# Kernel tuning notes

Measured on AMD Instinct MI355X. Metric: run time of the kernel, lower is better.

Reference implementation:

```python
import jax, jax.numpy as jnp
import numpy as np

BN_EPS = 1e-5

def bn(x, gamma, beta):
    # x: [N, C]; BatchNorm2d over (batch, spatial) == node axis here (training-mode batch stats)
    mu = x.mean(axis=0, keepdims=True)
    var = x.var(axis=0, keepdims=True)
    return (x - mu) * jax.lax.rsqrt(var + BN_EPS) * gamma + beta

def octree_conv(x, neigh, W):
    # x: [N, Cin]; neigh: [N, K] with values in [0, N], N == empty neighbor
    # W: [K, Cin, Cout]. Sparse octree conv = neighbor gather + contraction.
    xp = jnp.concatenate([x, jnp.zeros((1, x.shape[1]), x.dtype)], axis=0)  # zero row for empties
    g = xp[neigh]                                  # [N, K, Cin]
    return jnp.einsum('nkc,kcd->nd', g, W)         # [N, Cout]

def setup_inputs() -> dict:
    key = jax.random.key(0)
    ks = jax.random.split(key, 8)
    N, Cin, Cout, Cb, K = 60000, 256, 512, 128, 27
    s = 0.05
    return {
        'x': jax.random.normal(ks[0], (1, Cin, N, 1), jnp.float32),
        'neigh': jax.random.randint(ks[1], (N, K), 0, N + 1),
        'W1a': jax.random.normal(ks[2], (Cb, Cin), jnp.float32) * s,
        'g1a': jnp.ones((Cb,), jnp.float32), 'b1a': jnp.zeros((Cb,), jnp.float32),
        'W3': jax.random.normal(ks[3], (K, Cb, Cb), jnp.float32) * s,
        'g3': jnp.ones((Cb,), jnp.float32), 'b3': jnp.zeros((Cb,), jnp.float32),
        'W1b': jax.random.normal(ks[4], (Cout, Cb), jnp.float32) * s,
        'g1b': jnp.ones((Cout,), jnp.float32), 'b1b': jnp.zeros((Cout,), jnp.float32),
        'Wc': jax.random.normal(ks[5], (Cout, Cin), jnp.float32) * s,
        'gc': jnp.ones((Cout,), jnp.float32), 'bc': jnp.zeros((Cout,), jnp.float32),
    }

def reference(x, neigh, W1a, g1a, b1a, W3, g3, b3, W1b, g1b, b1b, Wc, gc, bc):
    h = jnp.squeeze(x, axis=(0, 3)).T                         # [N, Cin]
    c1 = jax.nn.relu(bn(h @ W1a.T, g1a, b1a))                 # 1x1 conv + BN + ReLU -> [N, Cb]
    c2 = jax.nn.relu(bn(octree_conv(c1, neigh, W3), g3, b3))  # sparse 3x3 octree conv + BN + ReLU
    c3 = bn(c2 @ W1b.T, g1b, b1b)                             # 1x1 conv + BN -> [N, Cout]
    sc = bn(h @ Wc.T, gc, bc)                                 # shortcut 1x1 conv + BN (Cin != Cout)
    out = jax.nn.relu(c3 + sc)
    return out.T[None, :, :, None]                            # [1, Cout, N, 1]
```

## Files before the change

kernel.cpp:

```cpp
#include <hip/hip_runtime.h>


typedef __bf16 bf16x8 __attribute__((ext_vector_type(8)));
typedef float f32x4 __attribute__((ext_vector_type(4)));
typedef unsigned short u16x8 __attribute__((ext_vector_type(8)));
typedef unsigned short u16x4 __attribute__((ext_vector_type(4)));

__device__ __forceinline__ unsigned short f2bfu(float f) {
  union { float f; unsigned u; } v; v.f = f;
  unsigned r = v.u + 0x7fffu + ((v.u >> 16) & 1u);
  return (unsigned short)(r >> 16);
}
__device__ __forceinline__ float bfu2f(unsigned short s) {
  union { unsigned u; float f; } v; v.u = ((unsigned)s) << 16;
  return v.f;
}

__device__ __forceinline__ void gload_lds16(const unsigned short* g, unsigned short* l) {
  __builtin_amdgcn_global_load_lds(
      (const __attribute__((address_space(1))) unsigned int*)(unsigned long long)g,
      (__attribute__((address_space(3))) unsigned int*)(unsigned int)(unsigned long long)l,
      16, 0, 0);
}

__device__ __forceinline__ int xcd_swz(int bid, int nwg) {
  int q = nwg >> 3, r = nwg & 7;
  int xcd = bid & 7, idx = bid >> 3;
  int base = xcd < r ? xcd * (q + 1) : r * (q + 1) + (xcd - r) * q;
  return base + idx;
}

__global__ __launch_bounds__(256) void prep_transpose(
    const float* __restrict__ x, unsigned short* __restrict__ h,
    const float* __restrict__ W1a, const float* __restrict__ W3,
    const float* __restrict__ W1b, const float* __restrict__ Wc,
    unsigned short* __restrict__ w1a, unsigned short* __restrict__ w3t,
    unsigned short* __restrict__ w1b, unsigned short* __restrict__ wc,
    int M, int MT) {
  __shared__ float tile[64][65];
  int t = threadIdx.x;
  if (blockIdx.x < 432) {
    int i = blockIdx.x * 256 + t;
    for (; i < 442368; i += 432 * 256) {
      if (i < 32768)  w1a[i] = f2bfu(W1a[i]);
      if (i < 65536)  w1b[i] = f2bfu(W1b[i]);
      if (i < 131072) wc[i]  = f2bfu(Wc[i]);
      int k = i >> 14, rr = i & 16383;
      int d = rr >> 7, c = rr & 127;
      w3t[i] = f2bfu(W3[(k << 14) + (c << 7) + d]);
    }
    return;
  }
  int bid = blockIdx.x - 432;
  int n0 = (bid % MT) * 64, c0 = (bid / MT) * 64;
  int nl = t & 63;
#pragma unroll
  for (int i = 0; i < 16; ++i) {
    int cl = i * 4 + (t >> 6);
    int n = n0 + nl;
    tile[cl][nl] = (n < M) ? x[(size_t)(c0 + cl) * M + n] : 0.f;
  }
  __syncthreads();
  int cl = t & 63;
#pragma unroll
  for (int i = 0; i < 16; ++i) {
    int nl2 = i * 4 + (t >> 6);
    int n = n0 + nl2;
    h[(size_t)n * 256 + c0 + cl] = f2bfu(tile[cl][nl2]);
  }
}

__global__ __launch_bounds__(512, 4) void gemm128(
    const unsigned short* __restrict__ A, const unsigned short* __restrict__ W,
    unsigned short* __restrict__ C, float* __restrict__ partials,
    int M, int Kd, int Nc, int ncol) {
  __shared__ unsigned short sA[2][128 * 64];
  __shared__ unsigned short sB[2][128 * 64];
  __shared__ float sStat[8][2][128];
  int t = threadIdx.x, wave = t >> 6, lane = t & 63;
  int flat = xcd_swz(blockIdx.x, gridDim.x);
  int n0 = (flat % ncol) * 128;
  int rowt = flat / ncol;
  int m0 = rowt * 128;
  int wr = wave >> 1, wcc = wave & 1;
  int l4 = lane >> 4, lc = lane & 15, lc7 = lc & 7;
  int lrow = lane >> 3, lch = lane & 7;
  f32x4 acc[2][4] = {};
  const int np = Kd >> 6;

  auto STAGE = [&](int p, int buf) {
    int k0 = p << 6;
#pragma unroll
    for (int i = 0; i < 2; ++i) {
      int row = wave * 16 + i * 8 + lrow;
      int sc = lch ^ (row & 7);
      gload_lds16(A + (size_t)(m0 + row) * Kd + k0 + sc * 8, &sA[buf][(wave * 16 + i * 8) * 64]);
    }
#pragma unroll
    for (int i = 0; i < 2; ++i) {
      int row = wave * 16 + i * 8 + lrow;
      int sc = lch ^ (row & 7);
      gload_lds16(W + (size_t)(n0 + row) * Kd + k0 + sc * 8, &sB[buf][(wave * 16 + i * 8) * 64]);
    }
  };
  auto COMPUTE = [&](int buf) {
#pragma unroll
    for (int kk = 0; kk < 2; ++kk) {
      bf16x8 af[2], bfr[4];
#pragma unroll
      for (int mi = 0; mi < 2; ++mi) {
        int row = wr * 32 + mi * 16 + lc;
        int chunk = (kk * 4 + l4) ^ lc7;
        af[mi] = __builtin_bit_cast(bf16x8, *(const u16x8*)(&sA[buf][row * 64 + chunk * 8]));
      }
#pragma unroll
      for (int ni = 0; ni < 4; ++ni) {
        int row = wcc * 64 + ni * 16 + lc;
        int chunk = (kk * 4 + l4) ^ lc7;
        bfr[ni] = __builtin_bit_cast(bf16x8, *(const u16x8*)(&sB[buf][row * 64 + chunk * 8]));
      }
      __builtin_amdgcn_s_setprio(1);
#pragma unroll
      for (int mi = 0; mi < 2; ++mi)
#pragma unroll
        for (int ni = 0; ni < 4; ++ni)
          acc[mi][ni] = __builtin_amdgcn_mfma_f32_16x16x32_bf16(af[mi], bfr[ni], acc[mi][ni], 0, 0, 0);
      __builtin_amdgcn_s_setprio(0);
    }
  };

  STAGE(0, 0);
  for (int p = 0; p < np; ++p) {
    int cur = p & 1;
    if (p < np - 1) {
      STAGE(p + 1, cur ^ 1);
      asm volatile("s_waitcnt vmcnt(4)" ::: "memory");
    } else {
      asm volatile("s_waitcnt vmcnt(0)" ::: "memory");
    }
    __builtin_amdgcn_sched_barrier(0);
    __builtin_amdgcn_s_barrier();
    __builtin_amdgcn_sched_barrier(0);
    COMPUTE(cur);
    __builtin_amdgcn_sched_barrier(0);
    __builtin_amdgcn_s_barrier();
  }

#pragma unroll
  for (int ni = 0; ni < 4; ++ni) {
    float s = 0.f, q = 0.f;
    int col = wcc * 64 + ni * 16 + lc;
#pragma unroll
    for (int mi = 0; mi < 2; ++mi)
#pragma unroll
      for (int j = 0; j < 4; ++j) {
        int n = m0 + wr * 32 + mi * 16 + l4 * 4 + j;
        unsigned short u = f2bfu(acc[mi][ni][j]);
        if (n < M) C[(size_t)n * Nc + n0 + col] = u;
        float v = bfu2f(u);
        s += v; q += v * v;
      }
    s += __shfl_xor(s, 16); s += __shfl_xor(s, 32);
    q += __shfl_xor(q, 16); q += __shfl_xor(q, 32);
    if (lane < 16) {
      sStat[wave][0][col] = s;
      sStat[wave][1][col] = q;
    }
  }
  __syncthreads();
  if (t < 128) {
    int wcs = t >> 6;
    float s = 0.f, q = 0.f;
#pragma unroll
    for (int g = 0; g < 4; ++g) {
      s += sStat[g * 2 + wcs][0][t];
      q += sStat[g * 2 + wcs][1][t];
    }
    partials[(size_t)rowt * (2 * Nc) + n0 + t] = s;
    partials[(size_t)rowt * (2 * Nc) + Nc + n0 + t] = q;
  }
}

__global__ __launch_bounds__(512, 4) void octree_sc(
    const unsigned short* __restrict__ c1, const int* __restrict__ neigh,
    const unsigned short* __restrict__ w3t, unsigned short* __restrict__ c2p,
    float* __restrict__ part12,
    const unsigned short* __restrict__ h, const unsigned short* __restrict__ wc,
    unsigned short* __restrict__ scp, float* __restrict__ partsc,
    int M, int MTO) {
  __shared__ unsigned short sA[2][128 * 64];
  __shared__ unsigned short sB[2][128 * 64];
  __shared__ union {
    unsigned short nidx[128 * 27];
    float stat[8][2][128];
  } u;
  int t = threadIdx.x, wave = t >> 6, lane = t & 63;
  int wr = wave >> 1, wcc = wave & 1;
  int l4 = lane >> 4, lc = lane & 15, lc7 = lc & 7;
  int lrow = lane >> 3, lch = lane & 7;
  f32x4 acc[2][4] = {};

  if (blockIdx.x < (unsigned)MTO) {
    int rowt = blockIdx.x;
    int m0 = rowt * 128;
    for (int i = t; i < 128 * 27; i += 512) {
      int row = i / 27;
      u.nidx[i] = (unsigned short)((m0 + row < M) ? neigh[(size_t)m0 * 27 + i] : M);
    }
    __syncthreads();

    auto STAGE = [&](int p, int buf) {
      int k = p >> 1, c0 = (p & 1) << 6;
#pragma unroll
      for (int i = 0; i < 2; ++i) {
        int row = wave * 16 + i * 8 + lrow;
        int nr = u.nidx[row * 27 + k];
        int sc = lch ^ (row & 7);
        gload_lds16(c1 + ((size_t)nr << 7) + c0 + sc * 8, &sA[buf][(wave * 16 + i * 8) * 64]);
      }
      const unsigned short* wk = w3t + ((size_t)k << 14);
#pragma unroll
      for (int i = 0; i < 2; ++i) {
        int row = wave * 16 + i * 8 + lrow;
        int sc = lch ^ (row & 7);
        gload_lds16(wk + ((size_t)row << 7) + c0 + sc * 8, &sB[buf][(wave * 16 + i * 8) * 64]);
      }
    };
    auto COMPUTE = [&](int buf) {
#pragma unroll
      for (int kk = 0; kk < 2; ++kk) {
        bf16x8 af[2], bfr[4];
#pragma unroll
        for (int mi = 0; mi < 2; ++mi) {
          int row = wr * 32 + mi * 16 + lc;
          int chunk = (kk * 4 + l4) ^ lc7;
          af[mi] = __builtin_bit_cast(bf16x8, *(const u16x8*)(&sA[buf][row * 64 + chunk * 8]));
        }
#pragma unroll
        for (int ni = 0; ni < 4; ++ni) {
          int row = wcc * 64 + ni * 16 + lc;
          int chunk = (kk * 4 + l4) ^ lc7;
          bfr[ni] = __builtin_bit_cast(bf16x8, *(const u16x8*)(&sB[buf][row * 64 + chunk * 8]));
        }
        __builtin_amdgcn_s_setprio(1);
#pragma unroll
        for (int mi = 0; mi < 2; ++mi)
#pragma unroll
          for (int ni = 0; ni < 4; ++ni)
            acc[mi][ni] = __builtin_amdgcn_mfma_f32_16x16x32_bf16(af[mi], bfr[ni], acc[mi][ni], 0, 0, 0);
        __builtin_amdgcn_s_setprio(0);
      }
    };

    STAGE(0, 0);
    for (int p = 0; p < 54; ++p) {
      int cur = p & 1;
      if (p < 53) {
        STAGE(p + 1, cur ^ 1);
        asm volatile("s_waitcnt vmcnt(4)" ::: "memory");
      } else {
        asm volatile("s_waitcnt vmcnt(0)" ::: "memory");
      }
      __builtin_amdgcn_sched_barrier(0);
      __builtin_amdgcn_s_barrier();
      __builtin_amdgcn_sched_barrier(0);
      COMPUTE(cur);
      __builtin_amdgcn_sched_barrier(0);
      __builtin_amdgcn_s_barrier();
    }

#pragma unroll
    for (int ni = 0; ni < 4; ++ni) {
      float s = 0.f, q = 0.f;
      int col = wcc * 64 + ni * 16 + lc;
#pragma unroll
      for (int mi = 0; mi < 2; ++mi)
#pragma unroll
        for (int j = 0; j < 4; ++j) {
          int n = m0 + wr * 32 + mi * 16 + l4 * 4 + j;
          unsigned short uo = f2bfu(acc[mi][ni][j]);
          if (n < M) c2p[(size_t)n * 128 + col] = uo;
          float v = bfu2f(uo);
          s += v; q += v * v;
        }
      s += __shfl_xor(s, 16); s += __shfl_xor(s, 32);
      q += __shfl_xor(q, 16); q += __shfl_xor(q, 32);
      if (lane < 16) {
        u.stat[wave][0][col] = s;
        u.stat[wave][1][col] = q;
      }
    }
    __syncthreads();
    if (t < 128) {
      int wcs = t >> 6;
      float s = 0.f, q = 0.f;
#pragma unroll
      for (int g = 0; g < 4; ++g) {
        s += u.stat[g * 2 + wcs][0][t];
        q += u.stat[g * 2 + wcs][1][t];
      }
      part12[(size_t)rowt * 256 + t] = s;
      part12[(size_t)rowt * 256 + 128 + t] = q;
    }
    return;
  }

  {
    int flat = xcd_swz(blockIdx.x - MTO, gridDim.x - MTO);
    int n0 = (flat & 3) * 128;
    int rowt = flat >> 2;
    int m0 = rowt * 128;

    auto STAGE = [&](int p, int buf) {
      int k0 = p << 6;
#pragma unroll
      for (int i = 0; i < 2; ++i) {
        int row = wave * 16 + i * 8 + lrow;
        int sc = lch ^ (row & 7);
        gload_lds16(h + (size_t)(m0 + row) * 256 + k0 + sc * 8, &sA[buf][(wave * 16 + i * 8) * 64]);
      }
#pragma unroll
      for (int i = 0; i < 2; ++i) {
        int row = wave * 16 + i * 8 + lrow;
        int sc = lch ^ (row & 7);
        gload_lds16(wc + (size_t)(n0 + row) * 256 + k0 + sc * 8, &sB[buf][(wave * 16 + i * 8) * 64]);
      }
    };
    auto COMPUTE = [&](int buf) {
#pragma unroll
      for (int kk = 0; kk < 2; ++kk) {
        bf16x8 af[2], bfr[4];
#pragma unroll
        for (int mi = 0; mi < 2; ++mi) {
          int row = wr * 32 + mi * 16 + lc;
          int chunk = (kk * 4 + l4) ^ lc7;
          af[mi] = __builtin_bit_cast(bf16x8, *(const u16x8*)(&sA[buf][row * 64 + chunk * 8]));
        }
#pragma unroll
        for (int ni = 0; ni < 4; ++ni) {
          int row = wcc * 64 + ni * 16 + lc;
          int chunk = (kk * 4 + l4) ^ lc7;
          bfr[ni] = __builtin_bit_cast(bf16x8, *(const u16x8*)(&sB[buf][row * 64 + chunk * 8]));
        }
        __builtin_amdgcn_s_setprio(1);
#pragma unroll
        for (int mi = 0; mi < 2; ++mi)
#pragma unroll
          for (int ni = 0; ni < 4; ++ni)
            acc[mi][ni] = __builtin_amdgcn_mfma_f32_16x16x32_bf16(af[mi], bfr[ni], acc[mi][ni], 0, 0, 0);
        __builtin_amdgcn_s_setprio(0);
      }
    };

    STAGE(0, 0);
    for (int p = 0; p < 4; ++p) {
      int cur = p & 1;
      if (p < 3) {
        STAGE(p + 1, cur ^ 1);
        asm volatile("s_waitcnt vmcnt(4)" ::: "memory");
      } else {
        asm volatile("s_waitcnt vmcnt(0)" ::: "memory");
      }
      __builtin_amdgcn_sched_barrier(0);
      __builtin_amdgcn_s_barrier();
      __builtin_amdgcn_sched_barrier(0);
      COMPUTE(cur);
      __builtin_amdgcn_sched_barrier(0);
      __builtin_amdgcn_s_barrier();
    }

#pragma unroll
    for (int ni = 0; ni < 4; ++ni) {
      float s = 0.f, q = 0.f;
      int col = wcc * 64 + ni * 16 + lc;
#pragma unroll
      for (int mi = 0; mi < 2; ++mi)
#pragma unroll
        for (int j = 0; j < 4; ++j) {
          int n = m0 + wr * 32 + mi * 16 + l4 * 4 + j;
          unsigned short uo = f2bfu(acc[mi][ni][j]);
          if (n < M) scp[(size_t)n * 512 + n0 + col] = uo;
          float v = bfu2f(uo);
          s += v; q += v * v;
        }
      s += __shfl_xor(s, 16); s += __shfl_xor(s, 32);
      q += __shfl_xor(q, 16); q += __shfl_xor(q, 32);
      if (lane < 16) {
        u.stat[wave][0][col] = s;
        u.stat[wave][1][col] = q;
      }
    }
    __syncthreads();
    if (t < 128) {
      int wcs = t >> 6;
      float s = 0.f, q = 0.f;
#pragma unroll
      for (int g = 0; g < 4; ++g) {
        s += u.stat[g * 2 + wcs][0][t];
        q += u.stat[g * 2 + wcs][1][t];
      }
      partsc[(size_t)rowt * 1024 + n0 + t] = s;
      partsc[(size_t)rowt * 1024 + 512 + n0 + t] = q;
    }
  }
}

__global__ __launch_bounds__(256) void bn_finalize(
    const float* __restrict__ partials, int nb, int C, int M,
    const float* __restrict__ g, const float* __restrict__ bt,
    float* __restrict__ ss) {
  int c = blockIdx.x;
  int t = threadIdx.x;
  float s = 0.f, s2 = 0.f;
  for (int b = t; b < nb; b += 256) {
    s += partials[(size_t)b * 2 * C + c];
    s2 += partials[(size_t)b * 2 * C + C + c];
  }
#pragma unroll
  for (int off = 32; off >= 1; off >>= 1) {
    s += __shfl_xor(s, off);
    s2 += __shfl_xor(s2, off);
  }
  __shared__ float sh[4][2];
  int wave = t >> 6, lane = t & 63;
  if (lane == 0) { sh[wave][0] = s; sh[wave][1] = s2; }
  __syncthreads();
  if (t == 0) {
    s = sh[0][0] + sh[1][0] + sh[2][0] + sh[3][0];
    s2 = sh[0][1] + sh[1][1] + sh[2][1] + sh[3][1];
    float mean = s / (float)M;
    float var = s2 / (float)M - mean * mean;
    float sc = g[c] * rsqrtf(var + 1e-5f);
    ss[c] = sc;
    ss[C + c] = bt[c] - mean * sc;
  }
}

__global__ __launch_bounds__(256) void bnrelu(
    const unsigned short* __restrict__ P, const float* __restrict__ ss,
    unsigned short* __restrict__ Aout, int total, int total2, int Cmask) {
  int i = (blockIdx.x * 256 + threadIdx.x) * 8;
  if (i >= total2) return;
  u16x8 o = {0, 0, 0, 0, 0, 0, 0, 0};
  if (i < total) {
    u16x8 v = *(const u16x8*)(P + i);
    int c0 = i & Cmask;
    int C = Cmask + 1;
#pragma unroll
    for (int j = 0; j < 8; ++j) {
      float f = bfu2f(v[j]) * ss[c0 + j] + ss[C + c0 + j];
      o[j] = f2bfu(fmaxf(f, 0.f));
    }
  }
  *(u16x8*)(Aout + i) = o;
}

__global__ __launch_bounds__(256) void final_out(
    const unsigned short* __restrict__ c3p, const unsigned short* __restrict__ scp,
    const float* __restrict__ ss3, const float* __restrict__ sssc,
    float* __restrict__ out, int M) {
  __shared__ float tile[64][129];
  int n0 = blockIdx.x * 64, c0 = blockIdx.y * 128;
  int t = threadIdx.x;
  int rowg = t >> 5, cg = (t & 31) * 4;
#pragma unroll
  for (int ps = 0; ps < 8; ++ps) {
    int nl = ps * 8 + rowg;
    int n = n0 + nl;
    float v0 = 0.f, v1 = 0.f, v2 = 0.f, v3 = 0.f;
    if (n < M) {
      u16x4 a = *(const u16x4*)(c3p + (size_t)n * 512 + c0 + cg);
      u16x4 b = *(const u16x4*)(scp + (size_t)n * 512 + c0 + cg);
      int c = c0 + cg;
      v0 = fmaxf(bfu2f(a[0]) * ss3[c + 0] + ss3[512 + c + 0] + bfu2f(b[0]) * sssc[c + 0] + sssc[512 + c + 0], 0.f);
      v1 = fmaxf(bfu2f(a[1]) * ss3[c + 1] + ss3[512 + c + 1] + bfu2f(b[1]) * sssc[c + 1] + sssc[512 + c + 1], 0.f);
      v2 = fmaxf(bfu2f(a[2]) * ss3[c + 2] + ss3[512 + c + 2] + bfu2f(b[2]) * sssc[c + 2] + sssc[512 + c + 2], 0.f);
      v3 = fmaxf(bfu2f(a[3]) * ss3[c + 3] + ss3[512 + c + 3] + bfu2f(b[3]) * sssc[c + 3] + sssc[512 + c + 3], 0.f);
    }
    tile[nl][cg + 0] = v0;
    tile[nl][cg + 1] = v1;
    tile[nl][cg + 2] = v2;
    tile[nl][cg + 3] = v3;
  }
  __syncthreads();
  int nl = t & 63, cq = t >> 6;
  int n = n0 + nl;
  if (n < M) {
#pragma unroll
    for (int i = 0; i < 32; ++i) {
      int cl = i * 4 + cq;
      out[(size_t)(c0 + cl) * M + n] = tile[nl][cl];
    }
  }
}

extern "C" void kernel_launch(void* const* d_in, const int* in_sizes, int n_in,
                              void* d_out, int out_size, void* d_ws, size_t ws_size,
                              hipStream_t stream) {
  const float* x   = (const float*)d_in[0];
  const int* neigh = (const int*)d_in[1];
  const float* W1a = (const float*)d_in[2];
  const float* g1a = (const float*)d_in[3];
  const float* b1a = (const float*)d_in[4];
  const float* W3  = (const float*)d_in[5];
  const float* g3  = (const float*)d_in[6];
  const float* b3  = (const float*)d_in[7];
  const float* W1b = (const float*)d_in[8];
  const float* g1b = (const float*)d_in[9];
  const float* b1b = (const float*)d_in[10];
  const float* Wc  = (const float*)d_in[11];
  const float* gc  = (const float*)d_in[12];
  const float* bc  = (const float*)d_in[13];
  float* out = (float*)d_out;

  const int M = in_sizes[1] / 27;
  const int MT = (M + 63) / 64;
  const int MTO = (M + 127) / 128;

  char* ws = (char*)d_ws;
  unsigned short* h   = (unsigned short*)(ws + 0);
  unsigned short* wA  = (unsigned short*)(ws + 30736384);
  unsigned short* wP  = (unsigned short*)(ws + 46104576);
  unsigned short* c3p = (unsigned short*)(ws + 61464576);
  unsigned short* scp = (unsigned short*)(ws + 122904576);
  unsigned short* w1a = (unsigned short*)(ws + 184344576);
  unsigned short* w3t = (unsigned short*)(ws + 184410112);
  unsigned short* w1b = (unsigned short*)(ws + 185294848);
  unsigned short* wc  = (unsigned short*)(ws + 185425920);
  float* ss1  = (float*)(ws + 185688064);
  float* ss2  = (float*)(ws + 185692160);
  float* ss3  = (float*)(ws + 185696256);
  float* sssc = (float*)(ws + 185700352);

  float* part1  = (float*)(ws + 61464576);
  float* part12 = (float*)(ws + 61464576 + 1048576);
  float* partsc = (float*)(ws + 61464576 + 2097152);
  float* part3  = (float*)wP;

  prep_transpose<<<432 + MT * 4, 256, 0, stream>>>(
      x, h, W1a, W3, W1b, Wc, w1a, w3t, w1b, wc, M, MT);

  const int total = M * 128, total2 = (MT * 64) * 128;
  const int bnGrid = (total2 / 8 + 255) / 256;

  gemm128<<<MTO, 512, 0, stream>>>(h, w1a, wP, part1, M, 256, 128, 1);
  bn_finalize<<<128, 256, 0, stream>>>(part1, MTO, 128, M, g1a, b1a, ss1);
  bnrelu<<<bnGrid, 256, 0, stream>>>(wP, ss1, wA, total, total2, 127);

  octree_sc<<<MTO + 4 * MTO, 512, 0, stream>>>(
      wA, neigh, w3t, wP, part12, h, wc, scp, partsc, M, MTO);
  bn_finalize<<<128, 256, 0, stream>>>(part12, MTO, 128, M, g3, b3, ss2);
  bn_finalize<<<512, 256, 0, stream>>>(partsc, MTO, 512, M, gc, bc, sssc);
  bnrelu<<<bnGrid, 256, 0, stream>>>(wP, ss2, wA, total, total2, 127);

  gemm128<<<4 * MTO, 512, 0, stream>>>(wA, w1b, c3p, part3, M, 128, 512, 4);
  bn_finalize<<<512, 256, 0, stream>>>(part3, MTO, 512, M, g1b, b1b, ss3);

  final_out<<<dim3(MT, 4), 256, 0, stream>>>(c3p, scp, ss3, sssc, out, M);
}
```

Before: 225.6 us.

## Compute c3 BN stats via Gram matrix and fuse final GEMM with shortcut

```diff
diff --git a/kernel.cpp b/kernel.cpp
--- a/kernel.cpp
+++ b/kernel.cpp
@@ -199,9 +199,11 @@
   int l4 = lane >> 4, lc = lane & 15, lc7 = lc & 7;
   int lrow = lane >> 3, lch = lane & 7;
   f32x4 acc[2][4] = {};
-
-  if (blockIdx.x < (unsigned)MTO) {
-    int rowt = blockIdx.x;
+  int bid = blockIdx.x;
+  bool isOct = (bid % 5) == 4;
+
+  if (isOct) {
+    int rowt = bid / 5;
     int m0 = rowt * 128;
     for (int i = t; i < 128 * 27; i += 512) {
       int row = i / 27;
@@ -306,7 +308,8 @@
   }
 
   {
-    int flat = xcd_swz(blockIdx.x - MTO, gridDim.x - MTO);
+    int scIdx = (bid / 5) * 4 + (bid % 5);
+    int flat = xcd_swz(scIdx, 4 * MTO);
     int n0 = (flat & 3) * 128;
     int rowt = flat >> 2;
     int m0 = rowt * 128;
@@ -455,42 +458,295 @@
   *(u16x8*)(Aout + i) = o;
 }
 
-__global__ __launch_bounds__(256) void final_out(
-    const unsigned short* __restrict__ c3p, const unsigned short* __restrict__ scp,
-    const float* __restrict__ ss3, const float* __restrict__ sssc,
+__global__ __launch_bounds__(256) void bnrelu2T(
+    const unsigned short* __restrict__ P, const float* __restrict__ ss,
+    unsigned short* __restrict__ wA, unsigned short* __restrict__ wAT,
+    int M, int Mpad) {
+  __shared__ unsigned short tp[128][72];
+  int t = threadIdx.x;
+  int n0 = blockIdx.x * 64;
+  int r = t >> 2, c0q = (t & 3) * 32;
+#pragma unroll
+  for (int q = 0; q < 4; ++q) {
+    int ch = c0q + q * 8;
+    u16x8 o = {0, 0, 0, 0, 0, 0, 0, 0};
+    if (n0 + r < M) {
+      u16x8 v = *(const u16x8*)(P + (size_t)(n0 + r) * 128 + ch);
+#pragma unroll
+      for (int j = 0; j < 8; ++j) {
+        float f = bfu2f(v[j]) * ss[ch + j] + ss[128 + ch + j];
+        o[j] = f2bfu(fmaxf(f, 0.f));
+      }
+    }
+    *(u16x8*)(wA + (size_t)(n0 + r) * 128 + ch) = o;
+#pragma unroll
+    for (int j = 0; j < 8; ++j) tp[ch + j][r] = o[j];
+  }
+  __syncthreads();
+  int c = t >> 1, half = t & 1;
+#pragma unroll
+  for (int i = 0; i < 4; ++i) {
+    u16x8 v = *(const u16x8*)(&tp[c][half * 32 + i * 8]);
+    *(u16x8*)(wAT + (size_t)c * Mpad + n0 + half * 32 + i * 8) = v;
+  }
+}
+
+__global__ __launch_bounds__(512, 4) void gram2(
+    const unsigned short* __restrict__ wAT, float* __restrict__ g2part,
+    int Mpad, int phasesTotal) {
+  __shared__ unsigned short sX[2][128 * 64];
+  int t = threadIdx.x, wave = t >> 6, lane = t & 63;
+  int wr = wave >> 2, wcc = wave & 3;
+  int l4 = lane >> 4, lc = lane & 15, lc7 = lc & 7;
+  int lrow = lane >> 3, lch = lane & 7;
+  int p0 = blockIdx.x * 4;
+  int pend = min(phasesTotal, p0 + 4);
+  f32x4 acc[4][2] = {};
+
+  auto STAGE = [&](int p, int buf) {
+#pragma unroll
+    for (int i = 0; i < 2; ++i) {
+      int row = wave * 16 + i * 8 + lrow;
+      int sc = lch ^ (row & 7);
+      gload_lds16(wAT + (size_t)row * Mpad + p * 64 + sc * 8, &sX[buf][(wave * 16 + i * 8) * 64]);
+    }
+  };
+  auto COMPUTE = [&](int buf) {
+#pragma unroll
+    for (int kk = 0; kk < 2; ++kk) {
+      bf16x8 af[4], bfr[2];
+#pragma unroll
+      for (int mi = 0; mi < 4; ++mi) {
+        int row = wr * 64 + mi * 16 + lc;
+        int chunk = (kk * 4 + l4) ^ lc7;
+        af[mi] = __builtin_bit_cast(bf16x8, *(const u16x8*)(&sX[buf][row * 64 + chunk * 8]));
+      }
+#pragma unroll
+      for (int ni = 0; ni < 2; ++ni) {
+        int row = wcc * 32 + ni * 16 + lc;
+        int chunk = (kk * 4 + l4) ^ lc7;
+        bfr[ni] = __builtin_bit_cast(bf16x8, *(const u16x8*)(&sX[buf][row * 64 + chunk * 8]));
+      }
+#pragma unroll
+      for (int mi = 0; mi < 4; ++mi)
+#pragma unroll
+        for (int ni = 0; ni < 2; ++ni)
+          acc[mi][ni] = __builtin_amdgcn_mfma_f32_16x16x32_bf16(af[mi], bfr[ni], acc[mi][ni], 0, 0, 0);
+    }
+  };
+
+  STAGE(p0, 0);
+  for (int p = p0; p < pend; ++p) {
+    int cur = (p - p0) & 1;
+    if (p + 1 < pend) {
+      STAGE(p + 1, cur ^ 1);
+      asm volatile("s_waitcnt vmcnt(2)" ::: "memory");
+    } else {
+      asm volatile("s_waitcnt vmcnt(0)" ::: "memory");
+    }
+    __builtin_amdgcn_sched_barrier(0);
+    __builtin_amdgcn_s_barrier();
+    __builtin_amdgcn_sched_barrier(0);
+    COMPUTE(cur);
+    __builtin_amdgcn_sched_barrier(0);
+    __builtin_amdgcn_s_barrier();
+  }
+
+  float* outp = g2part + (size_t)blockIdx.x * 16384;
+#pragma unroll
+  for (int mi = 0; mi < 4; ++mi)
+#pragma unroll
+    for (int ni = 0; ni < 2; ++ni) {
+      int col = wcc * 32 + ni * 16 + lc;
+#pragma unroll
+      for (int j = 0; j < 4; ++j) {
+        int row = wr * 64 + mi * 16 + l4 * 4 + j;
+        outp[row * 128 + col] = acc[mi][ni][j];
+      }
+    }
+}
+
+__global__ __launch_bounds__(256) void reduce_mean(
+    const float* __restrict__ g2part, int nk, float* __restrict__ G2,
+    const unsigned short* __restrict__ wAT, int Mpad, float* __restrict__ meansum) {
+  int b = blockIdx.x, t = threadIdx.x;
+  if (b < 64) {
+    int e = b * 256 + t;
+    float s = 0.f;
+    for (int k = 0; k < nk; ++k) s += g2part[(size_t)k * 16384 + e];
+    G2[e] = s;
+    return;
+  }
+  int r = b - 64;
+  float s = 0.f;
+  for (int cc = t * 8; cc < Mpad; cc += 2048) {
+    u16x8 v = *(const u16x8*)(wAT + (size_t)r * Mpad + cc);
+#pragma unroll
+    for (int j = 0; j < 8; ++j) s += bfu2f(v[j]);
+  }
+#pragma unroll
+  for (int off = 32; off >= 1; off >>= 1) s += __shfl_xor(s, off);
+  __shared__ float sh[4];
+  int wave = t >> 6, lane = t & 63;
+  if (lane == 0) sh[wave] = s;
+  __syncthreads();
+  if (t == 0) meansum[r] = sh[0] + sh[1] + sh[2] + sh[3];
+}
+
+__global__ __launch_bounds__(128) void qf_all(
+    const float* __restrict__ G2, const float* __restrict__ meansum,
+    const unsigned short* __restrict__ w1b, const float* __restrict__ g1b,
+    const float* __restrict__ b1b, const float* __restrict__ sssc,
+    float* __restrict__ sh3, unsigned short* __restrict__ w1bS,
+    unsigned short* __restrict__ Ddiag, int M) {
+  int j = blockIdx.x, i = threadIdx.x;
+  __shared__ float wsh[128];
+  __shared__ float red[4];
+  float wi = bfu2f(w1b[j * 128 + i]);
+  wsh[i] = wi;
+  __syncthreads();
+  float v = 0.f;
+  for (int l = 0; l < 128; ++l) v += G2[l * 128 + i] * wsh[l];
+  float a = wi * v;
+  float bmy = meansum[i] * wi;
+#pragma unroll
+  for (int off = 32; off >= 1; off >>= 1) {
+    a += __shfl_xor(a, off);
+    bmy += __shfl_xor(bmy, off);
+  }
+  int wv = i >> 6, ln = i & 63;
+  if (ln == 0) { red[wv * 2] = a; red[wv * 2 + 1] = bmy; }
+  __syncthreads();
+  float qf = red[0] + red[2];
+  float ms = red[1] + red[3];
+  float m3 = ms / (float)M;
+  float var = qf / (float)M - m3 * m3;
+  float s3 = g1b[j] * rsqrtf(var + 1e-5f);
+  if (i == 0) sh3[j] = b1b[j] - m3 * s3;
+  w1bS[j * 128 + i] = f2bfu(wi * s3);
+  Ddiag[j * 128 + i] = (i == (j & 127)) ? f2bfu(sssc[j]) : (unsigned short)0;
+}
+
+__global__ __launch_bounds__(512, 2) void final_fused(
+    const unsigned short* __restrict__ wA, const unsigned short* __restrict__ w1bS,
+    const unsigned short* __restrict__ scp, const unsigned short* __restrict__ Ddiag,
+    const float* __restrict__ sh3, const float* __restrict__ sssc,
     float* __restrict__ out, int M) {
-  __shared__ float tile[64][129];
-  int n0 = blockIdx.x * 64, c0 = blockIdx.y * 128;
-  int t = threadIdx.x;
-  int rowg = t >> 5, cg = (t & 31) * 4;
-#pragma unroll
-  for (int ps = 0; ps < 8; ++ps) {
-    int nl = ps * 8 + rowg;
-    int n = n0 + nl;
-    float v0 = 0.f, v1 = 0.f, v2 = 0.f, v3 = 0.f;
-    if (n < M) {
-      u16x4 a = *(const u16x4*)(c3p + (size_t)n * 512 + c0 + cg);
-      u16x4 b = *(const u16x4*)(scp + (size_t)n * 512 + c0 + cg);
-      int c = c0 + cg;
-      v0 = fmaxf(bfu2f(a[0]) * ss3[c + 0] + ss3[512 + c + 0] + bfu2f(b[0]) * sssc[c + 0] + sssc[512 + c + 0], 0.f);
-      v1 = fmaxf(bfu2f(a[1]) * ss3[c + 1] + ss3[512 + c + 1] + bfu2f(b[1]) * sssc[c + 1] + sssc[512 + c + 1], 0.f);
-      v2 = fmaxf(bfu2f(a[2]) * ss3[c + 2] + ss3[512 + c + 2] + bfu2f(b[2]) * sssc[c + 2] + sssc[512 + c + 2], 0.f);
-      v3 = fmaxf(bfu2f(a[3]) * ss3[c + 3] + ss3[512 + c + 3] + bfu2f(b[3]) * sssc[c + 3] + sssc[512 + c + 3], 0.f);
-    }
-    tile[nl][cg + 0] = v0;
-    tile[nl][cg + 1] = v1;
-    tile[nl][cg + 2] = v2;
-    tile[nl][cg + 3] = v3;
-  }
-  __syncthreads();
-  int nl = t & 63, cq = t >> 6;
-  int n = n0 + nl;
-  if (n < M) {
-#pragma unroll
-    for (int i = 0; i < 32; ++i) {
-      int cl = i * 4 + cq;
-      out[(size_t)(c0 + cl) * M + n] = tile[nl][cl];
-    }
+  __shared__ union {
+    struct { unsigned short A[2][128 * 64]; unsigned short B[2][128 * 64]; } m;
+    float tp[64][132];
+  } s;
+  int t = threadIdx.x, wave = t >> 6, lane = t & 63;
+  int wr = wave >> 1, wcc = wave & 1;
+  int l4 = lane >> 4, lc = lane & 15, lc7 = lc & 7;
+  int lrow = lane >> 3, lch = lane & 7;
+  int flat = xcd_swz(blockIdx.x, gridDim.x);
+  int n0 = (flat & 3) * 128;
+  int rowt = flat >> 2;
+  int m0 = rowt * 128;
+  f32x4 acc[2][4] = {};
+
+  auto STAGE = [&](int p, int buf) {
+#pragma unroll
+    for (int i = 0; i < 2; ++i) {
+      int row = wave * 16 + i * 8 + lrow;
+      int sc = lch ^ (row & 7);
+      const unsigned short* ap;
+      const unsigned short* bp;
+      if (p < 2) {
+        int k0 = p * 64;
+        ap = wA + (size_t)(m0 + row) * 128 + k0 + sc * 8;
+        bp = w1bS + (size_t)(n0 + row) * 128 + k0 + sc * 8;
+      } else {
+        int k0 = (p - 2) * 64;
+        ap = scp + (size_t)(m0 + row) * 512 + n0 + k0 + sc * 8;
+        bp = Ddiag + (size_t)(n0 + row) * 128 + k0 + sc * 8;
+      }
+      gload_lds16(ap, &s.m.A[buf][(wave * 16 + i * 8) * 64]);
+      gload_lds16(bp, &s.m.B[buf][(wave * 16 + i * 8) * 64]);
+    }
+  };
+  auto COMPUTE = [&](int buf) {
+#pragma unroll
+    for (int kk = 0; kk < 2; ++kk) {
+      bf16x8 af[2], bfr[4];
+#pragma unroll
+      for (int mi = 0; mi < 2; ++mi) {
+        int row = wr * 32 + mi * 16 + lc;
+        int chunk = (kk * 4 + l4) ^ lc7;
+        af[mi] = __builtin_bit_cast(bf16x8, *(const u16x8*)(&s.m.A[buf][row * 64 + chunk * 8]));
+      }
+#pragma unroll
+      for (int ni = 0; ni < 4; ++ni) {
+        int row = wcc * 64 + ni * 16 + lc;
+        int chunk = (kk * 4 + l4) ^ lc7;
+        bfr[ni] = __builtin_bit_cast(bf16x8, *(const u16x8*)(&s.m.B[buf][row * 64 + chunk * 8]));
+      }
+      __builtin_amdgcn_s_setprio(1);
+#pragma unroll
+      for (int mi = 0; mi < 2; ++mi)
+#pragma unroll
+        for (int ni = 0; ni < 4; ++ni)
+          acc[mi][ni] = __builtin_amdgcn_mfma_f32_16x16x32_bf16(af[mi], bfr[ni], acc[mi][ni], 0, 0, 0);
+      __builtin_amdgcn_s_setprio(0);
+    }
+  };
+
+  STAGE(0, 0);
+  for (int p = 0; p < 4; ++p) {
+    int cur = p & 1;
+    if (p < 3) {
+      STAGE(p + 1, cur ^ 1);
+      asm volatile("s_waitcnt vmcnt(4)" ::: "memory");
+    } else {
+      asm volatile("s_waitcnt vmcnt(0)" ::: "memory");
+    }
+    __builtin_amdgcn_sched_barrier(0);
+    __builtin_amdgcn_s_barrier();
+    __builtin_amdgcn_sched_barrier(0);
+    COMPUTE(cur);
+    __builtin_amdgcn_sched_barrier(0);
+    __builtin_amdgcn_s_barrier();
+  }
+
+#pragma unroll
+  for (int hf = 0; hf < 2; ++hf) {
+    if (wcc == hf) {
+#pragma unroll
+      for (int ni = 0; ni < 4; ++ni) {
+        int col_l = ni * 16 + lc;
+        int cg = n0 + hf * 64 + col_l;
+        float sh = sh3[cg] + sssc[512 + cg];
+#pragma unroll
+        for (int mi = 0; mi < 2; ++mi) {
+          f32x4 o;
+#pragma unroll
+          for (int j = 0; j < 4; ++j) o[j] = fmaxf(acc[mi][ni][j] + sh, 0.f);
+          *(f32x4*)(&s.tp[col_l][wr * 32 + mi * 16 + l4 * 4]) = o;
+        }
+      }
+    }
+    __syncthreads();
+    {
+      int col_l = t >> 3, seg = t & 7;
+      int cg = n0 + hf * 64 + col_l;
+      int nb = m0 + seg * 16;
+      f32x4 r0 = *(const f32x4*)(&s.tp[col_l][seg * 16 + 0]);
+      f32x4 r1 = *(const f32x4*)(&s.tp[col_l][seg * 16 + 4]);
+      f32x4 r2 = *(const f32x4*)(&s.tp[col_l][seg * 16 + 8]);
+      f32x4 r3 = *(const f32x4*)(&s.tp[col_l][seg * 16 + 12]);
+      if (nb + 16 <= M) {
+        f32x4* po = (f32x4*)(out + (size_t)cg * M + nb);
+        po[0] = r0; po[1] = r1; po[2] = r2; po[3] = r3;
+      } else {
+        float rr[16];
+        *(f32x4*)&rr[0] = r0; *(f32x4*)&rr[4] = r1;
+        *(f32x4*)&rr[8] = r2; *(f32x4*)&rr[12] = r3;
+        for (int e = 0; e < 16; ++e)
+          if (nb + e < M) out[(size_t)cg * M + nb + e] = rr[e];
+      }
+    }
+    __syncthreads();
   }
 }
 
@@ -516,12 +772,12 @@
   const int M = in_sizes[1] / 27;
   const int MT = (M + 63) / 64;
   const int MTO = (M + 127) / 128;
+  const int Mpad = MT * 64;
 
   char* ws = (char*)d_ws;
   unsigned short* h   = (unsigned short*)(ws + 0);
   unsigned short* wA  = (unsigned short*)(ws + 30736384);
   unsigned short* wP  = (unsigned short*)(ws + 46104576);
-  unsigned short* c3p = (unsigned short*)(ws + 61464576);
   unsigned short* scp = (unsigned short*)(ws + 122904576);
   unsigned short* w1a = (unsigned short*)(ws + 184344576);
   unsigned short* w3t = (unsigned short*)(ws + 184410112);
@@ -529,32 +785,43 @@
   unsigned short* wc  = (unsigned short*)(ws + 185425920);
   float* ss1  = (float*)(ws + 185688064);
   float* ss2  = (float*)(ws + 185692160);
-  float* ss3  = (float*)(ws + 185696256);
   float* sssc = (float*)(ws + 185700352);
 
-  float* part1  = (float*)(ws + 61464576);
-  float* part12 = (float*)(ws + 61464576 + 1048576);
-  float* partsc = (float*)(ws + 61464576 + 2097152);
-  float* part3  = (float*)wP;
+  const size_t O = 61464576;
+  float* part1   = (float*)(ws + O);
+  float* part12  = (float*)(ws + O + 1048576);
+  float* partsc  = (float*)(ws + O + 2097152);
+  float* g2part  = (float*)(ws + O + 4194304);
+  unsigned short* wAT = (unsigned short*)(ws + O + 22020096);
+  float* G2      = (float*)(ws + O + 39845888);
+  float* meansum = (float*)(ws + O + 39911424);
+  float* sh3     = (float*)(ws + O + 39913472);
+  unsigned short* w1bS  = (unsigned short*)(ws + O + 39915520);
+  unsigned short* Ddiag = (unsigned short*)(ws + O + 40046592);
 
   prep_transpose<<<432 + MT * 4, 256, 0, stream>>>(
       x, h, W1a, W3, W1b, Wc, w1a, w3t, w1b, wc, M, MT);
 
-  const int total = M * 128, total2 = (MT * 64) * 128;
+  const int total = M * 128, total2 = Mpad * 128;
   const int bnGrid = (total2 / 8 + 255) / 256;
 
   gemm128<<<MTO, 512, 0, stream>>>(h, w1a, wP, part1, M, 256, 128, 1);
   bn_finalize<<<128, 256, 0, stream>>>(part1, MTO, 128, M, g1a, b1a, ss1);
   bnrelu<<<bnGrid, 256, 0, stream>>>(wP, ss1, wA, total, total2, 127);
 
-  octree_sc<<<MTO + 4 * MTO, 512, 0, stream>>>(
+  octree_sc<<<5 * MTO, 512, 0, stream>>>(
       wA, neigh, w3t, wP, part12, h, wc, scp, partsc, M, MTO);
   bn_finalize<<<128, 256, 0, stream>>>(part12, MTO, 128, M, g3, b3, ss2);
   bn_finalize<<<512, 256, 0, stream>>>(partsc, MTO, 512, M, gc, bc, sssc);
-  bnrelu<<<bnGrid, 256, 0, stream>>>(wP, ss2, wA, total, total2, 127);
-
-  gemm128<<<4 * MTO, 512, 0, stream>>>(wA, w1b, c3p, part3, M, 128, 512, 4);
-  bn_finalize<<<512, 256, 0, stream>>>(part3, MTO, 512, M, g1b, b1b, ss3);
-
-  final_out<<<dim3(MT, 4), 256, 0, stream>>>(c3p, scp, ss3, sssc, out, M);
-}
+
+  bnrelu2T<<<MT, 256, 0, stream>>>(wP, ss2, wA, wAT, M, Mpad);
+
+  const int phases = Mpad / 64;
+  const int NK = (phases + 3) / 4;
+  gram2<<<NK, 512, 0, stream>>>(wAT, g2part, Mpad, phases);
+  reduce_mean<<<192, 256, 0, stream>>>(g2part, NK, G2, wAT, Mpad, meansum);
+  qf_all<<<512, 128, 0, stream>>>(G2, meansum, w1b, g1b, b1b, sssc,
+                                  sh3, w1bS, Ddiag, M);
+
+  final_fused<<<4 * MTO, 512, 0, stream>>>(wA, w1bS, scp, Ddiag, sh3, sssc, out, M);
+}
```

Measured after the change: 346.4 us. 53.5% more time.
